# Kernel tuning notes

Hardware: AMD Instinct MI355X
Metric: run time of the kernel (lower is better)

The kernel has to match this reference:

```python
import math
import jax, jax.numpy as jnp
import numpy as np

N_VARS = 10
K_MAX = 2
D = 32
B = 262144


def _fourier_emb(t, k_max=K_MAX):
    # [B, 1 + 2*k_max]: [1, cos(w t), sin(w t), cos(2 w t), sin(2 w t)]
    omega = 2.0 * math.pi
    feats = [jnp.ones_like(t)]
    for k in range(1, k_max + 1):
        feats.append(jnp.cos(k * omega * t))
        feats.append(jnp.sin(k * omega * t))
    return jnp.stack(feats, axis=-1)


def _make_mask(n_vars=N_VARS, mask_mode='th_only'):
    mask = jnp.eye(n_vars, dtype=jnp.float32)
    if mask_mode == 'th_only':
        mask = mask.at[:, 0].set(1.0)
        mask = mask.at[:, 1].set(1.0)
    else:
        mask = jnp.ones((n_vars, n_vars), dtype=jnp.float32)
    return mask


def setup_inputs() -> dict:
    key = jax.random.key(0)
    ks = jax.random.split(key, 8)
    x = jax.random.normal(ks[0], (B, N_VARS), dtype=jnp.float32)
    t_years = jax.random.uniform(ks[1], (B,), dtype=jnp.float32)
    n_basis = 1 + 2 * K_MAX
    # xavier-uniform-ish init for L_basis (fan over last two dims)
    limit = math.sqrt(6.0 / (N_VARS + N_VARS))
    L_basis = jax.random.uniform(ks[2], (n_basis, N_VARS, N_VARS), dtype=jnp.float32,
                                 minval=-limit, maxval=limit)
    wq = jax.random.normal(ks[3], (D,), dtype=jnp.float32)
    wk = jax.random.normal(ks[4], (D,), dtype=jnp.float32)
    wv = jax.random.normal(ks[5], (D,), dtype=jnp.float32)
    wo = jax.random.normal(ks[6], (D,), dtype=jnp.float32)
    alpha_w = 0.1 * jax.random.normal(ks[7], (n_basis,), dtype=jnp.float32)
    return {"x": x, "t_years": t_years, "L_basis": L_basis,
            "wq": wq, "wk": wk, "wv": wv, "wo": wo, "alpha_w": alpha_w}


def reference(x, t_years, L_basis, wq, wk, wv, wo, alpha_w):
    emb = _fourier_emb(t_years)                       # [B, K]
    L_t = jnp.einsum('bk,kuv->buv', emb, L_basis)      # [B, V, V]
    dxdt = jnp.einsum('buv,bv->bu', L_t, x)            # [B, V]

    # tokens: x[..., None] with Linear(1, d, bias=False) == outer product with weight vector
    Q = x[..., None] * wq                              # [B, V, D]
    K = x[..., None] * wk
    Vv = x[..., None] * wv

    scale = 1.0 / math.sqrt(D)
    scores = jnp.einsum('bvd,bud->bvu', Q, K) * scale  # [B, V, V]
    mask = _make_mask()
    scores = jnp.where(mask[None] < 0.5, -1e9, scores)
    attn = jax.nn.softmax(scores, axis=-1)
    O = jnp.einsum('bvu,bud->bvd', attn, Vv)           # [B, V, D]
    out = jnp.einsum('bvd,d->bv', O, wo)               # Wo: Linear(d,1,bias=False)

    alpha = jax.nn.sigmoid(emb @ alpha_w)              # [B]
    return dxdt + out * alpha[:, None]
```

## Files before the change

kernel.cpp:

```cpp
#include <hip/hip_runtime.h>
#include <math.h>

constexpr int NV  = 10;
constexpr int BLK = 256;

#define CONST_AS __attribute__((address_space(4)))
__device__ __forceinline__ const CONST_AS float* cptr(const float* p) {
    return (const CONST_AS float*)(unsigned long long)p;
}

__global__ __launch_bounds__(BLK, 4) void nxro_fused(
    const float* __restrict__ x,
    const float* __restrict__ t,
    const float* __restrict__ L,
    const float* __restrict__ wq,
    const float* __restrict__ wk,
    const float* __restrict__ wv,
    const float* __restrict__ wo,
    const float* __restrict__ aw,
    float* __restrict__ out,
    int B)
{
    const int tid  = threadIdx.x;
    const int lane = tid & 63;

    const long long b = (long long)blockIdx.x * BLK + tid;
    const bool act = (b < (long long)B);
    const long long bi = act ? b : 0;

    const float tt = t[bi];
    float2 p[5];
    {
        const float2* xr = reinterpret_cast<const float2*>(x + bi * NV);
        #pragma unroll
        for (int i = 0; i < 5; ++i) p[i] = xr[i];
    }

    float pa, pb;
    if (lane < 32) { pa = wq[lane];      pb = wk[lane];      }
    else           { pa = wv[lane - 32]; pb = wo[lane - 32]; }
    float dotv = pa * pb;
    #pragma unroll
    for (int m = 16; m >= 1; m >>= 1)
        dotv += __shfl_xor(dotv, m, 64);
    const float c = __shfl(dotv, 0, 64) * 0.17677669529663687f;
    const float g = __shfl(dotv, 32, 64);

    const float t2 = tt + tt;
    const float emb[5] = {
        1.f,
        __builtin_amdgcn_cosf(tt),
        __builtin_amdgcn_sinf(tt),
        __builtin_amdgcn_cosf(t2),
        __builtin_amdgcn_sinf(t2)
    };

    float xv[NV];
    #pragma unroll
    for (int i = 0; i < 5; ++i) { xv[2*i] = p[i].x; xv[2*i+1] = p[i].y; }

    float dxdt[NV];
    #pragma unroll
    for (int u = 0; u < NV; ++u) dxdt[u] = 0.f;
    {
        const float4* __restrict__ L4 = reinterpret_cast<const float4*>(L);
        #pragma unroll
        for (int k = 0; k < 5; ++k) {
            float zv[NV];
            const float ek = emb[k];
            #pragma unroll
            for (int v = 0; v < NV; ++v)
                zv[v] = (k == 0) ? xv[v] : ek * xv[v];
            #pragma unroll
            for (int f = 0; f < 25; ++f) {
                const float4 q = L4[k * 25 + f];
                #pragma unroll
                for (int cc = 0; cc < 4; ++cc) {
                    const int e = 100 * k + 4 * f + cc;
                    const int u = (e / 10) % 10;
                    const int v = e % 10;
                    const float qc = (cc == 0) ? q.x : (cc == 1) ? q.y
                                   : (cc == 2) ? q.z : q.w;
                    dxdt[u] = fmaf(qc, zv[v], dxdt[u]);
                }
            }
        }
    }

    const CONST_AS float* awc = cptr(aw);
    float zs = awc[0];
    zs = fmaf(emb[1], awc[1], zs);
    zs = fmaf(emb[2], awc[2], zs);
    zs = fmaf(emb[3], awc[3], zs);
    zs = fmaf(emb[4], awc[4], zs);
    const float ga = g * __builtin_amdgcn_rcpf(1.f + __expf(-zs));

    const float x0 = xv[0], x1 = xv[1];
    float res[NV];
    #pragma unroll
    for (int v = 0; v < NV; ++v) {
        const float s0 = xv[v] * x0 * c;
        const float s1 = xv[v] * x1 * c;
        float w;
        if (v < 2) {
            const float m = fmaxf(s0, s1);
            const float e0 = __expf(s0 - m), e1 = __expf(s1 - m);
            w = fmaf(e0, x0, e1 * x1) * __builtin_amdgcn_rcpf(e0 + e1);
        } else {
            const float sv = xv[v] * xv[v] * c;
            const float m = fmaxf(fmaxf(s0, s1), sv);
            const float e0 = __expf(s0 - m), e1 = __expf(s1 - m),
                        ev = __expf(sv - m);
            w = fmaf(e0, x0, fmaf(e1, x1, ev * xv[v]))
                * __builtin_amdgcn_rcpf(e0 + e1 + ev);
        }
        res[v] = fmaf(w, ga, dxdt[v]);
    }

    if (act) {
        float2* orow = reinterpret_cast<float2*>(out + b * NV);
        #pragma unroll
        for (int i = 0; i < 5; ++i)
            orow[i] = make_float2(res[2*i], res[2*i+1]);
    }
}

extern "C" void kernel_launch(void* const* d_in, const int* in_sizes, int n_in,
                              void* d_out, int out_size, void* d_ws, size_t ws_size,
                              hipStream_t stream) {
    const float* x  = (const float*)d_in[0];
    const float* t  = (const float*)d_in[1];
    const float* L  = (const float*)d_in[2];
    const float* wq = (const float*)d_in[3];
    const float* wk = (const float*)d_in[4];
    const float* wv = (const float*)d_in[5];
    const float* wo = (const float*)d_in[6];
    const float* aw = (const float*)d_in[7];
    float* out = (float*)d_out;
    const int B = in_sizes[1];

    const int grid = (B + BLK - 1) / BLK;
    nxro_fused<<<grid, BLK, 0, stream>>>(x, t, L, wq, wk, wv, wo, aw, out, B);
}
```

Measured before the change: 13.38 us.

## Split each row's output across two threads to halve per-thread work

Each row is now handled by two threads. Each thread computes five of the ten outputs, covering both the time-varying linear term and the attention term. The grid doubles, and launch bounds rise to 8 blocks per SM to allow more occupancy. In exchange, x, t, the Fourier features, the weight dots and the gate are computed twice per row, and the stores become partly unaligned scalar writes.

```diff
diff --git a/kernel.cpp b/kernel.cpp
--- a/kernel.cpp
+++ b/kernel.cpp
@@ -9,7 +9,64 @@
     return (const CONST_AS float*)(unsigned long long)p;
 }
 
-__global__ __launch_bounds__(BLK, 4) void nxro_fused(
+template<int H>
+__device__ __forceinline__ void dxdt_half(const float4* __restrict__ L4,
+                                          const float emb[5], const float xv[NV],
+                                          float dx[5]) {
+    #pragma unroll
+    for (int k = 0; k < 5; ++k) {
+        float zv[NV];
+        const float ek = emb[k];
+        #pragma unroll
+        for (int v = 0; v < NV; ++v)
+            zv[v] = (k == 0) ? xv[v] : ek * xv[v];
+        #pragma unroll
+        for (int j = 0; j < 13; ++j) {
+            const int qi = 25 * k + 12 * H + j;
+            const float4 q = L4[qi];
+            #pragma unroll
+            for (int cc = 0; cc < 4; ++cc) {
+                const int ed    = 4 * qi + cc;
+                const int local = ed - (100 * k + 50 * H);
+                if (local >= 0 && local < 50) {
+                    const int u = local / 10;
+                    const int v = local % 10;
+                    const float qc = (cc == 0) ? q.x : (cc == 1) ? q.y
+                                   : (cc == 2) ? q.z : q.w;
+                    dx[u] = fmaf(qc, zv[v], dx[u]);
+                }
+            }
+        }
+    }
+}
+
+template<int H>
+__device__ __forceinline__ void attn_half(const float xv[NV], const float dx[5],
+                                          float c, float ga, float res[5]) {
+    const float x0 = xv[0], x1 = xv[1];
+    #pragma unroll
+    for (int i = 0; i < 5; ++i) {
+        const int v = 5 * H + i;
+        const float s0 = xv[v] * x0 * c;
+        const float s1 = xv[v] * x1 * c;
+        float w;
+        if (v < 2) {
+            const float m = fmaxf(s0, s1);
+            const float e0 = __expf(s0 - m), e1 = __expf(s1 - m);
+            w = fmaf(e0, x0, e1 * x1) * __builtin_amdgcn_rcpf(e0 + e1);
+        } else {
+            const float sv = xv[v] * xv[v] * c;
+            const float m = fmaxf(fmaxf(s0, s1), sv);
+            const float e0 = __expf(s0 - m), e1 = __expf(s1 - m),
+                        ev = __expf(sv - m);
+            w = fmaf(e0, x0, fmaf(e1, x1, ev * xv[v]))
+                * __builtin_amdgcn_rcpf(e0 + e1 + ev);
+        }
+        res[i] = fmaf(w, ga, dx[i]);
+    }
+}
+
+__global__ __launch_bounds__(BLK, 8) void nxro_fused(
     const float* __restrict__ x,
     const float* __restrict__ t,
     const float* __restrict__ L,
@@ -23,15 +80,17 @@
 {
     const int tid  = threadIdx.x;
     const int lane = tid & 63;
+    const int rloc = tid & 127;
+    const int h    = tid >> 7;
 
-    const long long b = (long long)blockIdx.x * BLK + tid;
-    const bool act = (b < (long long)B);
-    const long long bi = act ? b : 0;
+    const long long row = (long long)blockIdx.x * 128 + rloc;
+    const bool act = (row < (long long)B);
+    const long long ri = act ? row : 0;
 
-    const float tt = t[bi];
+    const float tt = t[ri];
     float2 p[5];
     {
-        const float2* xr = reinterpret_cast<const float2*>(x + bi * NV);
+        const float2* xr = reinterpret_cast<const float2*>(x + ri * NV);
         #pragma unroll
         for (int i = 0; i < 5; ++i) p[i] = xr[i];
     }
@@ -59,34 +118,6 @@
     #pragma unroll
     for (int i = 0; i < 5; ++i) { xv[2*i] = p[i].x; xv[2*i+1] = p[i].y; }
 
-    float dxdt[NV];
-    #pragma unroll
-    for (int u = 0; u < NV; ++u) dxdt[u] = 0.f;
-    {
-        const float4* __restrict__ L4 = reinterpret_cast<const float4*>(L);
-        #pragma unroll
-        for (int k = 0; k < 5; ++k) {
-            float zv[NV];
-            const float ek = emb[k];
-            #pragma unroll
-            for (int v = 0; v < NV; ++v)
-                zv[v] = (k == 0) ? xv[v] : ek * xv[v];
-            #pragma unroll
-            for (int f = 0; f < 25; ++f) {
-                const float4 q = L4[k * 25 + f];
-                #pragma unroll
-                for (int cc = 0; cc < 4; ++cc) {
-                    const int e = 100 * k + 4 * f + cc;
-                    const int u = (e / 10) % 10;
-                    const int v = e % 10;
-                    const float qc = (cc == 0) ? q.x : (cc == 1) ? q.y
-                                   : (cc == 2) ? q.z : q.w;
-                    dxdt[u] = fmaf(qc, zv[v], dxdt[u]);
-                }
-            }
-        }
-    }
-
     const CONST_AS float* awc = cptr(aw);
     float zs = awc[0];
     zs = fmaf(emb[1], awc[1], zs);
@@ -95,33 +126,28 @@
     zs = fmaf(emb[4], awc[4], zs);
     const float ga = g * __builtin_amdgcn_rcpf(1.f + __expf(-zs));
 
-    const float x0 = xv[0], x1 = xv[1];
-    float res[NV];
-    #pragma unroll
-    for (int v = 0; v < NV; ++v) {
-        const float s0 = xv[v] * x0 * c;
-        const float s1 = xv[v] * x1 * c;
-        float w;
-        if (v < 2) {
-            const float m = fmaxf(s0, s1);
-            const float e0 = __expf(s0 - m), e1 = __expf(s1 - m);
-            w = fmaf(e0, x0, e1 * x1) * __builtin_amdgcn_rcpf(e0 + e1);
-        } else {
-            const float sv = xv[v] * xv[v] * c;
-            const float m = fmaxf(fmaxf(s0, s1), sv);
-            const float e0 = __expf(s0 - m), e1 = __expf(s1 - m),
-                        ev = __expf(sv - m);
-            w = fmaf(e0, x0, fmaf(e1, x1, ev * xv[v]))
-                * __builtin_amdgcn_rcpf(e0 + e1 + ev);
+    const float4* __restrict__ L4 = reinterpret_cast<const float4*>(L);
+    float dx[5] = {0.f, 0.f, 0.f, 0.f, 0.f};
+    float res[5];
+
+    if (h == 0) {
+        dxdt_half<0>(L4, emb, xv, dx);
+        attn_half<0>(xv, dx, c, ga, res);
+        if (act) {
+            float* op = out + row * NV;
+            *reinterpret_cast<float2*>(op)     = make_float2(res[0], res[1]);
+            *reinterpret_cast<float2*>(op + 2) = make_float2(res[2], res[3]);
+            op[4] = res[4];
         }
-        res[v] = fmaf(w, ga, dxdt[v]);
-    }
-
-    if (act) {
-        float2* orow = reinterpret_cast<float2*>(out + b * NV);
-        #pragma unroll
-        for (int i = 0; i < 5; ++i)
-            orow[i] = make_float2(res[2*i], res[2*i+1]);
+    } else {
+        dxdt_half<1>(L4, emb, xv, dx);
+        attn_half<1>(xv, dx, c, ga, res);
+        if (act) {
+            float* op = out + row * NV + 5;
+            op[0] = res[0];
+            *reinterpret_cast<float2*>(op + 1) = make_float2(res[1], res[2]);
+            *reinterpret_cast<float2*>(op + 3) = make_float2(res[3], res[4]);
+        }
     }
 }
 
@@ -139,6 +165,7 @@
     float* out = (float*)d_out;
     const int B = in_sizes[1];
 
-    const int grid = (B + BLK - 1) / BLK;
+    const int rowsPerBlk = 128;
+    const int grid = (B + rowsPerBlk - 1) / rowsPerBlk;
     nxro_fused<<<grid, BLK, 0, stream>>>(x, t, L, wq, wk, wv, wo, aw, out, B);
 }
```

Result: faster. 13.06 us (median of 3 runs) (-2.4%).
